# Performance work log

Hardware: AMD Instinct MI355X
Metric: run time of the kernel (lower is better)

Reference implementation:

```python
import jax, jax.numpy as jnp
import numpy as np


def setup_inputs() -> dict:
    key = jax.random.key(0)
    B, C, T = 64, 256, 2048
    X = jax.random.normal(key, (B, C, T), dtype=jnp.float32)
    return {"X": X}


def reference(X) -> jnp.ndarray:
    # torch.cov(correction=0) per sample: rows = variables, cols = observations
    T = X.shape[-1]
    Xc = X - jnp.mean(X, axis=-1, keepdims=True)      # [B, C, T]
    cov = jnp.einsum('bct,bdt->bcd', Xc, Xc) / T       # [B, C, C]
    return cov
```

## Files before the change

kernel.cpp:

```cpp
#include <hip/hip_runtime.h>


#define NB 64
#define NC 256
#define NT 2048
#define KITER 32

typedef __bf16 bf16x8 __attribute__((ext_vector_type(8)));
typedef float  f32x8  __attribute__((ext_vector_type(8)));
typedef float  f32x4  __attribute__((ext_vector_type(4)));

__global__ __launch_bounds__(128, 2) void cov_kernel(const float* __restrict__ X,
                                                     float* __restrict__ out) {
    const int bid  = blockIdx.x;
    const int xcd  = bid & 7;
    const int s    = bid >> 3;
    const int b    = xcd + 8 * (s / 10);
    const int tile = s % 10;
    int tm, tn;
    if (tile < 4)      { tm = 0; tn = tile; }
    else if (tile < 7) { tm = 1; tn = tile - 3; }
    else if (tile < 9) { tm = 2; tn = tile - 5; }
    else               { tm = 3; tn = 3; }
    const int row0 = tm * 64, col0 = tn * 64;

    const float* __restrict__ Xb = X + (size_t)b * (NC * NT);

    const int t    = threadIdx.x;
    const int lane = t & 63;
    const int wave = t >> 6;
    const int quad = lane >> 4;
    const int l16  = lane & 15;

    const float* baseA = Xb + (size_t)(row0 + l16) * NT + wave * (NT / 2) + quad * 8;
    const float* baseB = Xb + (size_t)(col0 + l16) * NT + wave * (NT / 2) + quad * 8;

    f32x4 acc[4][4], accRS[4], accCS[4];
#pragma unroll
    for (int i = 0; i < 4; ++i) {
        accRS[i] = (f32x4){0.f, 0.f, 0.f, 0.f};
        accCS[i] = (f32x4){0.f, 0.f, 0.f, 0.f};
#pragma unroll
        for (int j = 0; j < 4; ++j) acc[i][j] = (f32x4){0.f, 0.f, 0.f, 0.f};
    }

    const bf16x8 ones = {(__bf16)1.0f, (__bf16)1.0f, (__bf16)1.0f, (__bf16)1.0f,
                         (__bf16)1.0f, (__bf16)1.0f, (__bf16)1.0f, (__bf16)1.0f};

    f32x8 vA[4], vB[4];
#pragma unroll
    for (int i = 0; i < 4; ++i) {
        vA[i] = *(const f32x8*)(baseA + (size_t)i * 16 * NT);
        vB[i] = *(const f32x8*)(baseB + (size_t)i * 16 * NT);
    }

#pragma unroll 1
    for (int it = 0; it < KITER; ++it) {
        bf16x8 aF[4], bF[4];
#pragma unroll
        for (int i = 0; i < 4; ++i) {
            aF[i] = __builtin_convertvector(vA[i], bf16x8);
            bF[i] = __builtin_convertvector(vB[i], bf16x8);
        }
        if (it + 1 < KITER) {
            const int off = (it + 1) * 32;
#pragma unroll
            for (int i = 0; i < 4; ++i) {
                vA[i] = *(const f32x8*)(baseA + (size_t)i * 16 * NT + off);
                vB[i] = *(const f32x8*)(baseB + (size_t)i * 16 * NT + off);
            }
        }
#pragma unroll
        for (int mt = 0; mt < 4; ++mt) {
            accRS[mt] = __builtin_amdgcn_mfma_f32_16x16x32_bf16(aF[mt], ones, accRS[mt], 0, 0, 0);
#pragma unroll
            for (int nt = 0; nt < 4; ++nt)
                acc[mt][nt] = __builtin_amdgcn_mfma_f32_16x16x32_bf16(aF[mt], bF[nt], acc[mt][nt], 0, 0, 0);
        }
#pragma unroll
        for (int nt = 0; nt < 4; ++nt)
            accCS[nt] = __builtin_amdgcn_mfma_f32_16x16x32_bf16(ones, bF[nt], accCS[nt], 0, 0, 0);
    }

    __shared__ float red[64 * 65];
    __shared__ float rsum[64];
    __shared__ float csum[64];

    if (wave == 0) {
#pragma unroll
        for (int mt = 0; mt < 4; ++mt)
#pragma unroll
            for (int nt = 0; nt < 4; ++nt)
#pragma unroll
                for (int r = 0; r < 4; ++r)
                    red[(mt * 16 + quad * 4 + r) * 65 + nt * 16 + l16] = acc[mt][nt][r];
        if (l16 == 0) {
#pragma unroll
            for (int mt = 0; mt < 4; ++mt)
#pragma unroll
                for (int r = 0; r < 4; ++r)
                    rsum[mt * 16 + quad * 4 + r] = accRS[mt][r];
        }
        if (quad == 0) {
#pragma unroll
            for (int nt = 0; nt < 4; ++nt)
                csum[nt * 16 + l16] = accCS[nt][0];
        }
    }
    __syncthreads();

    if (wave == 1) {
        const float invT = 1.0f / NT;
        float* __restrict__ outB = out + (size_t)b * (NC * NC);
#pragma unroll
        for (int mt = 0; mt < 4; ++mt) {
#pragma unroll
            for (int nt = 0; nt < 4; ++nt) {
#pragma unroll
                for (int r = 0; r < 4; ++r) {
                    const int rl = mt * 16 + quad * 4 + r;
                    const int cl = nt * 16 + l16;
                    const float tot = red[rl * 65 + cl] + acc[mt][nt][r];
                    const float rsT = rsum[rl] + accRS[mt][r];
                    const float csT = csum[cl] + accCS[nt][0];
                    const float val = (tot - rsT * csT * invT) * invT;
                    outB[(size_t)(row0 + rl) * NC + (col0 + cl)] = val;
                    outB[(size_t)(col0 + cl) * NC + (row0 + rl)] = val;
                }
            }
        }
    }
}

extern "C" void kernel_launch(void* const* d_in, const int* in_sizes, int n_in,
                              void* d_out, int out_size, void* d_ws, size_t ws_size,
                              hipStream_t stream) {
    const float* X = (const float*)d_in[0];
    float* out = (float*)d_out;
    (void)in_sizes; (void)n_in; (void)out_size; (void)d_ws; (void)ws_size;
    cov_kernel<<<640, 128, 0, stream>>>(X, out);
}
```

Before: 240.9 us.

## Stage bf16 tiles in LDS with 128x128 block tiles and 8-wave split-K

Replaces the per-wave direct global-to-register loads over 64x64 triangle tiles with 128x128 output tiles per block, each block holding 8 waves (4 spatial quadrants times 2 K-halves). Global fp32 data is converted to bf16 and written into double-buffered LDS, so each row is loaded from global memory once per block and shared across waves. This drops the symmetric-triangle trick, so every output tile is computed instead of being mirrored, and a barrier is added per iteration. The intent is to cut redundant global traffic and raise occupancy; the price is extra MFMA work on the off-diagonal tiles plus synchronisation overhead.

```diff
diff --git a/kernel.cpp b/kernel.cpp
--- a/kernel.cpp
+++ b/kernel.cpp
@@ -4,36 +4,47 @@
 #define NB 64
 #define NC 256
 #define NT 2048
-#define KITER 32
+#define NITER 32
 
 typedef __bf16 bf16x8 __attribute__((ext_vector_type(8)));
 typedef float  f32x8  __attribute__((ext_vector_type(8)));
 typedef float  f32x4  __attribute__((ext_vector_type(4)));
 
-__global__ __launch_bounds__(128, 2) void cov_kernel(const float* __restrict__ X,
+__global__ __launch_bounds__(512, 2) void cov_kernel(const float* __restrict__ X,
                                                      float* __restrict__ out) {
+    __shared__ __align__(16) unsigned char smem[68608];
+    __bf16* sAB  = (__bf16*)smem;
+    float*  redF = (float*)smem;
+
     const int bid  = blockIdx.x;
     const int xcd  = bid & 7;
-    const int s    = bid >> 3;
-    const int b    = xcd + 8 * (s / 10);
-    const int tile = s % 10;
-    int tm, tn;
-    if (tile < 4)      { tm = 0; tn = tile; }
-    else if (tile < 7) { tm = 1; tn = tile - 3; }
-    else if (tile < 9) { tm = 2; tn = tile - 5; }
-    else               { tm = 3; tn = 3; }
-    const int row0 = tm * 64, col0 = tn * 64;
+    const int g    = bid >> 3;
+    const int b    = xcd + 8 * (g >> 2);
+    const int q    = g & 3;
+    const int row0 = (q >> 1) * 128, col0 = (q & 1) * 128;
 
     const float* __restrict__ Xb = X + (size_t)b * (NC * NT);
 
     const int t    = threadIdx.x;
     const int lane = t & 63;
     const int wave = t >> 6;
+    const int h    = wave >> 2;
+    const int wq   = wave & 3;
+    const int wm   = wq >> 1, wn = wq & 1;
     const int quad = lane >> 4;
     const int l16  = lane & 15;
 
-    const float* baseA = Xb + (size_t)(row0 + l16) * NT + wave * (NT / 2) + quad * 8;
-    const float* baseB = Xb + (size_t)(col0 + l16) * NT + wave * (NT / 2) + quad * 8;
+    const int u  = t & 255;
+    const int sr = u >> 2;
+    const int sc = (u & 3) * 8;
+    const float* gA0 = Xb + (size_t)(row0 + sr) * NT + h * (NT / 2) + sc;
+    const float* gA1 = gA0 + (size_t)64 * NT;
+    const float* gB0 = Xb + (size_t)(col0 + sr) * NT + h * (NT / 2) + sc;
+    const float* gB1 = gB0 + (size_t)64 * NT;
+
+    __bf16* sA[2] = { sAB + (0 * 2 + h) * 4096, sAB + (1 * 2 + h) * 4096 };
+    __bf16* sB[2] = { sAB + 16384 + (0 * 2 + h) * 4096, sAB + 16384 + (1 * 2 + h) * 4096 };
+    const int woff = sr * 32 + sc;
 
     f32x4 acc[4][4], accRS[4], accCS[4];
 #pragma unroll
@@ -43,33 +54,51 @@
 #pragma unroll
         for (int j = 0; j < 4; ++j) acc[i][j] = (f32x4){0.f, 0.f, 0.f, 0.f};
     }
-
     const bf16x8 ones = {(__bf16)1.0f, (__bf16)1.0f, (__bf16)1.0f, (__bf16)1.0f,
                          (__bf16)1.0f, (__bf16)1.0f, (__bf16)1.0f, (__bf16)1.0f};
 
-    f32x8 vA[4], vB[4];
-#pragma unroll
-    for (int i = 0; i < 4; ++i) {
-        vA[i] = *(const f32x8*)(baseA + (size_t)i * 16 * NT);
-        vB[i] = *(const f32x8*)(baseB + (size_t)i * 16 * NT);
-    }
+    f32x8 pA0 = *(const f32x8*)gA0;
+    f32x8 pA1 = *(const f32x8*)gA1;
+    f32x8 pB0 = *(const f32x8*)gB0;
+    f32x8 pB1 = *(const f32x8*)gB1;
+    *(bf16x8*)(sA[0] + woff)        = __builtin_convertvector(pA0, bf16x8);
+    *(bf16x8*)(sA[0] + woff + 2048) = __builtin_convertvector(pA1, bf16x8);
+    *(bf16x8*)(sB[0] + woff)        = __builtin_convertvector(pB0, bf16x8);
+    *(bf16x8*)(sB[0] + woff + 2048) = __builtin_convertvector(pB1, bf16x8);
+    pA0 = *(const f32x8*)(gA0 + 32);
+    pA1 = *(const f32x8*)(gA1 + 32);
+    pB0 = *(const f32x8*)(gB0 + 32);
+    pB1 = *(const f32x8*)(gB1 + 32);
+    __syncthreads();
 
-#pragma unroll 1
-    for (int it = 0; it < KITER; ++it) {
+    const int aBase = (wm * 64 + l16) * 32 + quad * 8;
+    const int bBase = (wn * 64 + l16) * 32 + quad * 8;
+
+#pragma unroll 2
+    for (int k = 0; k < NITER; ++k) {
+        const int cur = k & 1, nxt = cur ^ 1;
+
+        if (k + 1 < NITER) {
+            *(bf16x8*)(sA[nxt] + woff)        = __builtin_convertvector(pA0, bf16x8);
+            *(bf16x8*)(sA[nxt] + woff + 2048) = __builtin_convertvector(pA1, bf16x8);
+            *(bf16x8*)(sB[nxt] + woff)        = __builtin_convertvector(pB0, bf16x8);
+            *(bf16x8*)(sB[nxt] + woff + 2048) = __builtin_convertvector(pB1, bf16x8);
+        }
+        if (k + 2 < NITER) {
+            pA0 = *(const f32x8*)(gA0 + (k + 2) * 32);
+            pA1 = *(const f32x8*)(gA1 + (k + 2) * 32);
+            pB0 = *(const f32x8*)(gB0 + (k + 2) * 32);
+            pB1 = *(const f32x8*)(gB1 + (k + 2) * 32);
+        }
+
         bf16x8 aF[4], bF[4];
 #pragma unroll
-        for (int i = 0; i < 4; ++i) {
-            aF[i] = __builtin_convertvector(vA[i], bf16x8);
-            bF[i] = __builtin_convertvector(vB[i], bf16x8);
-        }
-        if (it + 1 < KITER) {
-            const int off = (it + 1) * 32;
+        for (int mt = 0; mt < 4; ++mt)
+            aF[mt] = *(const bf16x8*)(sA[cur] + aBase + mt * 16 * 32);
 #pragma unroll
-            for (int i = 0; i < 4; ++i) {
-                vA[i] = *(const f32x8*)(baseA + (size_t)i * 16 * NT + off);
-                vB[i] = *(const f32x8*)(baseB + (size_t)i * 16 * NT + off);
-            }
-        }
+        for (int nt = 0; nt < 4; ++nt)
+            bF[nt] = *(const bf16x8*)(sB[cur] + bBase + nt * 16 * 32);
+
 #pragma unroll
         for (int mt = 0; mt < 4; ++mt) {
             accRS[mt] = __builtin_amdgcn_mfma_f32_16x16x32_bf16(aF[mt], ones, accRS[mt], 0, 0, 0);
@@ -80,13 +109,15 @@
 #pragma unroll
         for (int nt = 0; nt < 4; ++nt)
             accCS[nt] = __builtin_amdgcn_mfma_f32_16x16x32_bf16(ones, bF[nt], accCS[nt], 0, 0, 0);
+
+        __syncthreads();
     }
 
-    __shared__ float red[64 * 65];
-    __shared__ float rsum[64];
-    __shared__ float csum[64];
+    float* red = redF + wq * (64 * 65);
+    float* rs  = redF + 4 * (64 * 65);
+    float* cs  = rs + 256;
 
-    if (wave == 0) {
+    if (h == 1) {
 #pragma unroll
         for (int mt = 0; mt < 4; ++mt)
 #pragma unroll
@@ -99,17 +130,17 @@
             for (int mt = 0; mt < 4; ++mt)
 #pragma unroll
                 for (int r = 0; r < 4; ++r)
-                    rsum[mt * 16 + quad * 4 + r] = accRS[mt][r];
+                    rs[wq * 64 + mt * 16 + quad * 4 + r] = accRS[mt][r];
         }
         if (quad == 0) {
 #pragma unroll
             for (int nt = 0; nt < 4; ++nt)
-                csum[nt * 16 + l16] = accCS[nt][0];
+                cs[wq * 64 + nt * 16 + l16] = accCS[nt][0];
         }
     }
     __syncthreads();
 
-    if (wave == 1) {
+    if (h == 0) {
         const float invT = 1.0f / NT;
         float* __restrict__ outB = out + (size_t)b * (NC * NC);
 #pragma unroll
@@ -118,14 +149,13 @@
             for (int nt = 0; nt < 4; ++nt) {
 #pragma unroll
                 for (int r = 0; r < 4; ++r) {
-                    const int rl = mt * 16 + quad * 4 + r;
-                    const int cl = nt * 16 + l16;
-                    const float tot = red[rl * 65 + cl] + acc[mt][nt][r];
-                    const float rsT = rsum[rl] + accRS[mt][r];
-                    const float csT = csum[cl] + accCS[nt][0];
-                    const float val = (tot - rsT * csT * invT) * invT;
-                    outB[(size_t)(row0 + rl) * NC + (col0 + cl)] = val;
-                    outB[(size_t)(col0 + cl) * NC + (row0 + rl)] = val;
+                    const int R = mt * 16 + quad * 4 + r;
+                    const int C = nt * 16 + l16;
+                    const float tot = red[R * 65 + C] + acc[mt][nt][r];
+                    const float Sx  = rs[wq * 64 + R] + accRS[mt][r];
+                    const float Sy  = cs[wq * 64 + C] + accCS[nt][0];
+                    outB[(size_t)(row0 + wm * 64 + R) * NC + (col0 + wn * 64 + C)] =
+                        (tot - Sx * Sy * invT) * invT;
                 }
             }
         }
@@ -138,5 +168,5 @@
     const float* X = (const float*)d_in[0];
     float* out = (float*)d_out;
     (void)in_sizes; (void)n_in; (void)out_size; (void)d_ws; (void)ws_size;
-    cov_kernel<<<640, 128, 0, stream>>>(X, out);
+    cov_kernel<<<256, 512, 0, stream>>>(X, out);
 }
```

Result: faster. 205.4 us (-14.7%).
